# Kernel optimization log

Hardware: AMD Instinct MI355X
Metric: run time of the kernel (lower is better)

Reference implementation:

```python
import jax, jax.numpy as jnp
import numpy as np

N_NODES = 50000
N_EDGES = 640000
D = 128
L = 3
LN_EPS = 1e-5


def _layer_norm(x, g, b):
    mu = jnp.mean(x, axis=-1, keepdims=True)
    var = jnp.mean(jnp.square(x - mu), axis=-1, keepdims=True)
    return (x - mu) * jax.lax.rsqrt(var + LN_EPS) * g + b


def setup_inputs() -> dict:
    key = jax.random.key(0)
    ks = jax.random.split(key, 8)
    scale = 1.0 / np.sqrt(D)
    x = jax.random.normal(ks[0], (N_NODES, D), dtype=jnp.float32)
    edge_index = jax.random.randint(ks[1], (2, N_EDGES), 0, N_NODES, dtype=jnp.int32)
    return {
        "x": x,
        "edge_index": edge_index,
        "eps": jnp.zeros((L,), jnp.float32),  # GIN epsilon, init 0.0
        "W1": jax.random.normal(ks[2], (L, D, D), jnp.float32) * scale,
        "b1": jnp.zeros((L, D), jnp.float32),
        "W2": jax.random.normal(ks[3], (L, D, D), jnp.float32) * scale,
        "b2": jnp.zeros((L, D), jnp.float32),
        "ln_g": jnp.ones((L, D), jnp.float32),   # per-conv LayerNorm
        "ln_b": jnp.zeros((L, D), jnp.float32),
        "skip_g": jnp.ones((L - 1, D), jnp.float32),  # outer norms for layers 0..L-2
        "skip_b": jnp.zeros((L - 1, D), jnp.float32),
    }


def reference(x, edge_index, eps, W1, b1, W2, b2, ln_g, ln_b, skip_g, skip_b):
    src = edge_index[0]
    dst = edge_index[1]
    h = x  # no input_norm (use_input_norm=False)
    for i in range(L):
        h_in = h
        # scatter-add neighbor aggregation: out[dst] += h[src]
        agg = jax.ops.segment_sum(h[src], dst, num_segments=N_NODES)
        z = (1.0 + eps[i]) * h + agg
        # 2-layer MLP: Linear -> ReLU -> Linear
        z = jnp.maximum(z @ W1[i] + b1[i], 0.0) @ W2[i] + b2[i]
        z = _layer_norm(z, ln_g[i], ln_b[i])
        if i < L - 1:
            z = _layer_norm(z, skip_g[i], skip_b[i])  # skip-path norm
            z = jnp.maximum(z, 0.0)  # ReLU; dropout is identity in eval
        h = z + h_in  # residual (shapes always match: in==hidden)
    return h
```

## Files before the change

### kernel.cpp

```cpp
#include <hip/hip_runtime.h>
#include <hip/hip_bf16.h>

#define N_NODES 50000
#define N_EDGES 640000
#define D 128
#define NPAD 50048
#define LAYERS 3
#define SCAN_NB 196

typedef __attribute__((ext_vector_type(4))) float f32x4;
typedef __attribute__((ext_vector_type(8))) short bf16x8;
typedef __attribute__((ext_vector_type(4))) short bf16x4;

static __device__ __forceinline__ short f2bf(float f) {
    union { float f; unsigned u; } x; x.f = f;
    unsigned r = x.u + 0x7fffu + ((x.u >> 16) & 1u);
    return (short)(r >> 16);
}
static __device__ __forceinline__ float bf2f(short s) {
    union { unsigned u; float f; } x; x.u = ((unsigned)(unsigned short)s) << 16;
    return x.f;
}

__global__ void init_kernel(const f32x4* __restrict__ in, bf16x4* __restrict__ hb) {
    int t = blockIdx.x * 256 + threadIdx.x;
    f32x4 v = in[t];
    bf16x4 p; p[0] = f2bf(v.x); p[1] = f2bf(v.y); p[2] = f2bf(v.z); p[3] = f2bf(v.w);
    hb[t] = p;
}

__global__ void prepw_kernel(const float* __restrict__ W1, const float* __restrict__ W2,
                             short* __restrict__ wt) {
    int t = blockIdx.x * 256 + threadIdx.x;
    if (t >= 6 * 16384) return;
    int m = t >> 14, rem = t & 16383;
    int c = rem >> 7, k = rem & 127;
    const float* src = (m < 3) ? (W1 + m * 16384) : (W2 + (m - 3) * 16384);
    wt[m * 16384 + c * 128 + k] = f2bf(src[k * 128 + c]);
}

__global__ void hist_kernel(const int* __restrict__ dst, int* __restrict__ deg) {
    int e = blockIdx.x * 256 + threadIdx.x;
    if (e < N_EDGES) atomicAdd(&deg[dst[e]], 1);
}

__global__ void scan1_kernel(const int* __restrict__ deg, int* __restrict__ rs,
                             int* __restrict__ bsum) {
    __shared__ int tmp[256];
    int i = blockIdx.x * 256 + threadIdx.x;
    int v = (i < N_NODES) ? deg[i] : 0;
    tmp[threadIdx.x] = v;
    __syncthreads();
    for (int off = 1; off < 256; off <<= 1) {
        int t = (threadIdx.x >= off) ? tmp[threadIdx.x - off] : 0;
        __syncthreads();
        tmp[threadIdx.x] += t;
        __syncthreads();
    }
    if (i < N_NODES) rs[i] = tmp[threadIdx.x] - v;
    if (threadIdx.x == 255) bsum[blockIdx.x] = tmp[255];
}

__global__ void scan2_kernel(int* __restrict__ bsum) {
    __shared__ int tmp[256];
    int v = (threadIdx.x < SCAN_NB) ? bsum[threadIdx.x] : 0;
    tmp[threadIdx.x] = v;
    __syncthreads();
    for (int off = 1; off < 256; off <<= 1) {
        int t = (threadIdx.x >= off) ? tmp[threadIdx.x - off] : 0;
        __syncthreads();
        tmp[threadIdx.x] += t;
        __syncthreads();
    }
    if (threadIdx.x < SCAN_NB) bsum[threadIdx.x] = tmp[threadIdx.x] - v;
}

__global__ void scan3_kernel(int* __restrict__ rs, const int* __restrict__ bsum) {
    int i = blockIdx.x * 256 + threadIdx.x;
    if (i < N_NODES) rs[i] += bsum[blockIdx.x];
}

__global__ void fill_kernel(const int* __restrict__ src, const int* __restrict__ dst,
                            const int* __restrict__ rs, int* __restrict__ cursor,
                            int* __restrict__ col) {
    int e = blockIdx.x * 256 + threadIdx.x;
    if (e >= N_EDGES) return;
    int d = dst[e];
    int p = atomicAdd(&cursor[d], 1);
    col[rs[d] + p] = src[e];
}

__global__ __launch_bounds__(256) void agg_kernel(const bf16x8* __restrict__ hb,
                                                  const int* __restrict__ rs,
                                                  const int* __restrict__ deg,
                                                  const int* __restrict__ col,
                                                  const float* __restrict__ epsArr, int layer,
                                                  bf16x8* __restrict__ z) {
    int t = blockIdx.x * 256 + threadIdx.x;
    int node = t >> 4, lane = t & 15;
    if (node >= NPAD) return;
    bf16x8 o;
    if (node < N_NODES) {
        float acc[8] = {0.f, 0.f, 0.f, 0.f, 0.f, 0.f, 0.f, 0.f};
        int start = rs[node], dg = deg[node];
        const int* cp = col + start;
        int base = 0;
        for (; base + 4 <= dg; base += 4) {
            int c0 = cp[base], c1 = cp[base + 1], c2 = cp[base + 2], c3 = cp[base + 3];
            bf16x8 v0 = hb[(size_t)c0 * 16 + lane];
            bf16x8 v1 = hb[(size_t)c1 * 16 + lane];
            bf16x8 v2 = hb[(size_t)c2 * 16 + lane];
            bf16x8 v3 = hb[(size_t)c3 * 16 + lane];
#pragma unroll
            for (int e = 0; e < 8; ++e)
                acc[e] += (bf2f(v0[e]) + bf2f(v1[e])) + (bf2f(v2[e]) + bf2f(v3[e]));
        }
        for (; base < dg; ++base) {
            bf16x8 v = hb[(size_t)cp[base] * 16 + lane];
#pragma unroll
            for (int e = 0; e < 8; ++e) acc[e] += bf2f(v[e]);
        }
        float s = 1.0f + epsArr[layer];
        bf16x8 hv = hb[(size_t)node * 16 + lane];
#pragma unroll
        for (int e = 0; e < 8; ++e) o[e] = f2bf(fmaf(s, bf2f(hv[e]), acc[e]));
    } else {
        o = (bf16x8)(short)0;
    }
    z[(size_t)node * 16 + lane] = o;
}

template <bool LAST>
__global__ __launch_bounds__(256, 2) void mlp_kernel(const short* __restrict__ Z,
                                                     const short* __restrict__ Wt1,
                                                     const float* __restrict__ B1,
                                                     const short* __restrict__ Wt2,
                                                     const float* __restrict__ B2,
                                                     const float* __restrict__ G1,
                                                     const float* __restrict__ Bt1,
                                                     const float* __restrict__ G2,
                                                     const float* __restrict__ Bt2,
                                                     const float* __restrict__ RS,
                                                     float* __restrict__ H,
                                                     short* __restrict__ HB) {
    __shared__ __align__(16) char lds[49152 + 3072];
    const int t = threadIdx.x;
    const int wave = t >> 6, lane = t & 63;
    const int r = lane & 15, kq = lane >> 4;
    const int lrow = wave * 16 + r;
    const int row = blockIdx.x * 64 + lrow;
    const int swzr = (r & 7) << 4;
    const int swzl = (lrow & 7) << 4;
    const int fcol = kq * 16;

    const short* Zr = Z + (size_t)row * D + kq * 8;
    bf16x8 zb0 = *(const bf16x8*)(Zr);
    bf16x8 zb1 = *(const bf16x8*)(Zr + 32);
    bf16x8 zb2 = *(const bf16x8*)(Zr + 64);
    bf16x8 zb3 = *(const bf16x8*)(Zr + 96);
    __builtin_amdgcn_sched_barrier(0);

    bf16x8 g2[8];
    {
        bf16x8 g1[8];
#pragma unroll
        for (int i = 0; i < 8; ++i) g1[i] = *(const bf16x8*)(Wt1 + i * 2048 + t * 8);
#pragma unroll
        for (int i = 0; i < 8; ++i) g2[i] = *(const bf16x8*)(Wt2 + i * 2048 + t * 8);
        if (t < (LAST ? 128 : 192)) {
            int which = t >> 5, chunk = t & 31;
            const float* vp = (which == 0) ? B1 : (which == 1) ? B2 : (which == 2) ? G1
                            : (which == 3) ? Bt1 : (which == 4) ? G2 : Bt2;
            *(f32x4*)(lds + 49152 + which * 512 + chunk * 16) = *(const f32x4*)(vp + chunk * 4);
        }
#pragma unroll
        for (int i = 0; i < 8; ++i) {
            int b = i * 4096 + t * 16;
            *(bf16x8*)(lds + (b ^ (((b >> 8) & 7) << 4))) = g1[i];
        }
    }
    __syncthreads();

    bf16x4 p[8];
#pragma unroll
    for (int ct = 0; ct < 8; ++ct) {
        int wb = (ct * 16 + r) * 256 + kq * 16;
        f32x4 acc = {0.f, 0.f, 0.f, 0.f};
        acc = __builtin_amdgcn_mfma_f32_16x16x32_bf16(*(const bf16x8*)(lds + ((wb      ) ^ swzr)), zb0, acc, 0, 0, 0);
        acc = __builtin_amdgcn_mfma_f32_16x16x32_bf16(*(const bf16x8*)(lds + ((wb +  64) ^ swzr)), zb1, acc, 0, 0, 0);
        acc = __builtin_amdgcn_mfma_f32_16x16x32_bf16(*(const bf16x8*)(lds + ((wb + 128) ^ swzr)), zb2, acc, 0, 0, 0);
        acc = __builtin_amdgcn_mfma_f32_16x16x32_bf16(*(const bf16x8*)(lds + ((wb + 192) ^ swzr)), zb3, acc, 0, 0, 0);
        f32x4 bias = *(const f32x4*)(lds + 49152 + 0 + ct * 64 + fcol);
        p[ct][0] = f2bf(fmaxf(acc[0] + bias.x, 0.0f));
        p[ct][1] = f2bf(fmaxf(acc[1] + bias.y, 0.0f));
        p[ct][2] = f2bf(fmaxf(acc[2] + bias.z, 0.0f));
        p[ct][3] = f2bf(fmaxf(acc[3] + bias.w, 0.0f));
    }
    __syncthreads();

    f32x4 rsv[8] = {};
    if (row < N_NODES) {
#pragma unroll
        for (int ct = 0; ct < 8; ++ct)
            rsv[ct] = *(const f32x4*)(RS + (size_t)row * D + ct * 16 + kq * 4);
    }
    __builtin_amdgcn_sched_barrier(0);

#pragma unroll
    for (int i = 0; i < 8; ++i) {
        int b = i * 4096 + t * 16;
        *(bf16x8*)(lds + (b ^ (((b >> 8) & 7) << 4))) = g2[i];
    }
#pragma unroll
    for (int ct = 0; ct < 8; ++ct)
        *(bf16x4*)(lds + 32768 + ((lrow * 256 + ct * 32 + kq * 8) ^ swzl)) = p[ct];
    __syncthreads();

    bf16x8 hb0 = *(const bf16x8*)(lds + 32768 + ((lrow * 256 +   0 + kq * 16) ^ swzl));
    bf16x8 hb1 = *(const bf16x8*)(lds + 32768 + ((lrow * 256 +  64 + kq * 16) ^ swzl));
    bf16x8 hb2 = *(const bf16x8*)(lds + 32768 + ((lrow * 256 + 128 + kq * 16) ^ swzl));
    bf16x8 hb3 = *(const bf16x8*)(lds + 32768 + ((lrow * 256 + 192 + kq * 16) ^ swzl));

    f32x4 o[8];
#pragma unroll
    for (int ct = 0; ct < 8; ++ct) {
        int wb = (ct * 16 + r) * 256 + kq * 16;
        f32x4 acc = {0.f, 0.f, 0.f, 0.f};
        acc = __builtin_amdgcn_mfma_f32_16x16x32_bf16(*(const bf16x8*)(lds + ((wb      ) ^ swzr)), hb0, acc, 0, 0, 0);
        acc = __builtin_amdgcn_mfma_f32_16x16x32_bf16(*(const bf16x8*)(lds + ((wb +  64) ^ swzr)), hb1, acc, 0, 0, 0);
        acc = __builtin_amdgcn_mfma_f32_16x16x32_bf16(*(const bf16x8*)(lds + ((wb + 128) ^ swzr)), hb2, acc, 0, 0, 0);
        acc = __builtin_amdgcn_mfma_f32_16x16x32_bf16(*(const bf16x8*)(lds + ((wb + 192) ^ swzr)), hb3, acc, 0, 0, 0);
        f32x4 bias = *(const f32x4*)(lds + 49152 + 512 + ct * 64 + fcol);
        o[ct] = acc + bias;
    }

    float s = 0.f, q = 0.f;
#pragma unroll
    for (int ct = 0; ct < 8; ++ct) {
        s += o[ct].x + o[ct].y + o[ct].z + o[ct].w;
        q += o[ct].x * o[ct].x + o[ct].y * o[ct].y + o[ct].z * o[ct].z + o[ct].w * o[ct].w;
    }
    s += __shfl_xor(s, 16, 64); q += __shfl_xor(q, 16, 64);
    s += __shfl_xor(s, 32, 64); q += __shfl_xor(q, 32, 64);
    float mu = s * (1.0f / D);
    float rstd = rsqrtf(q * (1.0f / D) - mu * mu + 1e-5f);
#pragma unroll
    for (int ct = 0; ct < 8; ++ct) {
        f32x4 g = *(const f32x4*)(lds + 49152 + 1024 + ct * 64 + fcol);
        f32x4 b = *(const f32x4*)(lds + 49152 + 1536 + ct * 64 + fcol);
        o[ct] = (o[ct] - mu) * rstd * g + b;
    }

    if (!LAST) {
        float s2 = 0.f, q2 = 0.f;
#pragma unroll
        for (int ct = 0; ct < 8; ++ct) {
            s2 += o[ct].x + o[ct].y + o[ct].z + o[ct].w;
            q2 += o[ct].x * o[ct].x + o[ct].y * o[ct].y + o[ct].z * o[ct].z + o[ct].w * o[ct].w;
        }
        s2 += __shfl_xor(s2, 16, 64); q2 += __shfl_xor(q2, 16, 64);
        s2 += __shfl_xor(s2, 32, 64); q2 += __shfl_xor(q2, 32, 64);
        float mu2 = s2 * (1.0f / D);
        float rstd2 = rsqrtf(q2 * (1.0f / D) - mu2 * mu2 + 1e-5f);
#pragma unroll
        for (int ct = 0; ct < 8; ++ct) {
            f32x4 g = *(const f32x4*)(lds + 49152 + 2048 + ct * 64 + fcol);
            f32x4 b = *(const f32x4*)(lds + 49152 + 2560 + ct * 64 + fcol);
            f32x4 y = (o[ct] - mu2) * rstd2 * g + b;
            y.x = fmaxf(y.x, 0.f); y.y = fmaxf(y.y, 0.f);
            y.z = fmaxf(y.z, 0.f); y.w = fmaxf(y.w, 0.f);
            o[ct] = y;
        }
    }

    if (row < N_NODES) {
#pragma unroll
        for (int ct = 0; ct < 8; ++ct) {
            size_t off = (size_t)row * D + ct * 16 + kq * 4;
            f32x4 hv = rsv[ct] + o[ct];
            *(f32x4*)(H + off) = hv;
            if (!LAST) {
                bf16x4 pb;
                pb[0] = f2bf(hv.x); pb[1] = f2bf(hv.y); pb[2] = f2bf(hv.z); pb[3] = f2bf(hv.w);
                *(bf16x4*)(HB + off) = pb;
            }
        }
    }
}

extern "C" void kernel_launch(void* const* d_in, const int* in_sizes, int n_in,
                              void* d_out, int out_size, void* d_ws, size_t ws_size,
                              hipStream_t stream) {
    const float* x   = (const float*)d_in[0];
    const int*   ei  = (const int*)d_in[1];
    const float* eps = (const float*)d_in[2];
    const float* W1  = (const float*)d_in[3];
    const float* b1  = (const float*)d_in[4];
    const float* W2  = (const float*)d_in[5];
    const float* b2  = (const float*)d_in[6];
    const float* lng = (const float*)d_in[7];
    const float* lnb = (const float*)d_in[8];
    const float* skg = (const float*)d_in[9];
    const float* skb = (const float*)d_in[10];
    float* h = (float*)d_out;

    char* ws = (char*)d_ws;
    short* zbuf = (short*)ws;
    short* hbb  = (short*)(ws + 12812288);
    short* wt   = (short*)(ws + 25624576);
    int*   rs   = (int*)  (ws + 25821184);
    int*   deg  = (int*)  (ws + 26021376);
    int*   cur  = (int*)  (ws + 26221568);
    int*   col  = (int*)  (ws + 26421760);
    int*   bsum = (int*)  (ws + 28981760);

    const int* srcIdx = ei;
    const int* dstIdx = ei + N_EDGES;

    init_kernel<<<(N_NODES * 32) / 256, 256, 0, stream>>>((const f32x4*)x, (bf16x4*)hbb);
    prepw_kernel<<<(6 * 16384) / 256, 256, 0, stream>>>(W1, W2, wt);

    hipMemsetAsync(deg, 0, 2 * 200192, stream);
    hist_kernel<<<(N_EDGES + 255) / 256, 256, 0, stream>>>(dstIdx, deg);
    scan1_kernel<<<SCAN_NB, 256, 0, stream>>>(deg, rs, bsum);
    scan2_kernel<<<1, 256, 0, stream>>>(bsum);
    scan3_kernel<<<SCAN_NB, 256, 0, stream>>>(rs, bsum);
    fill_kernel<<<(N_EDGES + 255) / 256, 256, 0, stream>>>(srcIdx, dstIdx, rs, cur, col);

    for (int l = 0; l < LAYERS; ++l) {
        agg_kernel<<<NPAD / 16, 256, 0, stream>>>(
            (const bf16x8*)hbb, rs, deg, col, eps, l, (bf16x8*)zbuf);
        const float* rsrc = (l == 0) ? x : h;
        if (l < LAYERS - 1) {
            mlp_kernel<false><<<NPAD / 64, 256, 0, stream>>>(
                zbuf, wt + l * 16384, b1 + l * D, wt + (3 + l) * 16384, b2 + l * D,
                lng + l * D, lnb + l * D, skg + l * D, skb + l * D, rsrc, h, hbb);
        } else {
            mlp_kernel<true><<<NPAD / 64, 256, 0, stream>>>(
                zbuf, wt + l * 16384, b1 + l * D, wt + (3 + l) * 16384, b2 + l * D,
                lng + l * D, lnb + l * D, nullptr, nullptr, rsrc, h, nullptr);
        }
    }
}
```

Measured before the change: 224.4 us.

## Split bf16 node features into four column slabs for cache-local gather

Node features and aggregation output now live in four 32-column slabs instead of full 128-column rows. Consecutive aggregation blocks are interleaved across slabs, each handling one slab for 64 nodes with four lanes per node. This is meant to shrink the working set of random neighbor gathers so more of each slab stays in L2/MALL. The gather loop is also unrolled to eight neighbors. The cost is four separate gathers of col and rs/deg per node, and producer/consumer kernels that write and read the strided slab layout.

After: 226.7 us. About the same (+1.0%).

```diff
diff --git a/kernel.cpp b/kernel.cpp
--- a/kernel.cpp
+++ b/kernel.cpp
@@ -8,6 +8,9 @@
 #define LAYERS 3
 #define SCAN_NB 196
 
+#define SLAB_HB (N_NODES * 32)
+#define SLAB_Z  (NPAD * 32)
+
 typedef __attribute__((ext_vector_type(4))) float f32x4;
 typedef __attribute__((ext_vector_type(8))) short bf16x8;
 typedef __attribute__((ext_vector_type(4))) short bf16x4;
@@ -22,11 +25,18 @@
     return x.f;
 }
 
-__global__ void init_kernel(const f32x4* __restrict__ in, bf16x4* __restrict__ hb) {
+__global__ void init_kernel(const float* __restrict__ x, short* __restrict__ hb) {
     int t = blockIdx.x * 256 + threadIdx.x;
-    f32x4 v = in[t];
-    bf16x4 p; p[0] = f2bf(v.x); p[1] = f2bf(v.y); p[2] = f2bf(v.z); p[3] = f2bf(v.w);
-    hb[t] = p;
+    if (t >= N_NODES * 16) return;
+    int node = t >> 4, fg = t & 15;
+    int s = fg >> 2, w = (fg & 3) * 8;
+    const float* xp = x + (size_t)node * D + fg * 8;
+    f32x4 a = *(const f32x4*)(xp);
+    f32x4 b = *(const f32x4*)(xp + 4);
+    bf16x8 p;
+    p[0] = f2bf(a.x); p[1] = f2bf(a.y); p[2] = f2bf(a.z); p[3] = f2bf(a.w);
+    p[4] = f2bf(b.x); p[5] = f2bf(b.y); p[6] = f2bf(b.z); p[7] = f2bf(b.w);
+    *(bf16x8*)(hb + (size_t)s * SLAB_HB + (size_t)node * 32 + w) = p;
 }
 
 __global__ void prepw_kernel(const float* __restrict__ W1, const float* __restrict__ W2,
@@ -90,44 +100,53 @@
     col[rs[d] + p] = src[e];
 }
 
-__global__ __launch_bounds__(256) void agg_kernel(const bf16x8* __restrict__ hb,
+__global__ __launch_bounds__(256) void agg_kernel(const short* __restrict__ hb,
                                                   const int* __restrict__ rs,
                                                   const int* __restrict__ deg,
                                                   const int* __restrict__ col,
                                                   const float* __restrict__ epsArr, int layer,
-                                                  bf16x8* __restrict__ z) {
-    int t = blockIdx.x * 256 + threadIdx.x;
-    int node = t >> 4, lane = t & 15;
-    if (node >= NPAD) return;
+                                                  short* __restrict__ z) {
+    int b = blockIdx.x;
+    int j = b & 7, m = b >> 3;
+    int slice = j & 3;
+    int chunk = 2 * m + (j >> 2);
+    int t = threadIdx.x;
+    int g = t >> 2, lane4 = t & 3;
+    int node = chunk * 64 + g;
+    const short* tab = hb + (size_t)slice * SLAB_HB;
     bf16x8 o;
     if (node < N_NODES) {
         float acc[8] = {0.f, 0.f, 0.f, 0.f, 0.f, 0.f, 0.f, 0.f};
         int start = rs[node], dg = deg[node];
         const int* cp = col + start;
         int base = 0;
-        for (; base + 4 <= dg; base += 4) {
-            int c0 = cp[base], c1 = cp[base + 1], c2 = cp[base + 2], c3 = cp[base + 3];
-            bf16x8 v0 = hb[(size_t)c0 * 16 + lane];
-            bf16x8 v1 = hb[(size_t)c1 * 16 + lane];
-            bf16x8 v2 = hb[(size_t)c2 * 16 + lane];
-            bf16x8 v3 = hb[(size_t)c3 * 16 + lane];
+        for (; base + 8 <= dg; base += 8) {
+            bf16x8 v0 = *(const bf16x8*)(tab + (size_t)cp[base + 0] * 32 + lane4 * 8);
+            bf16x8 v1 = *(const bf16x8*)(tab + (size_t)cp[base + 1] * 32 + lane4 * 8);
+            bf16x8 v2 = *(const bf16x8*)(tab + (size_t)cp[base + 2] * 32 + lane4 * 8);
+            bf16x8 v3 = *(const bf16x8*)(tab + (size_t)cp[base + 3] * 32 + lane4 * 8);
+            bf16x8 v4 = *(const bf16x8*)(tab + (size_t)cp[base + 4] * 32 + lane4 * 8);
+            bf16x8 v5 = *(const bf16x8*)(tab + (size_t)cp[base + 5] * 32 + lane4 * 8);
+            bf16x8 v6 = *(const bf16x8*)(tab + (size_t)cp[base + 6] * 32 + lane4 * 8);
+            bf16x8 v7 = *(const bf16x8*)(tab + (size_t)cp[base + 7] * 32 + lane4 * 8);
 #pragma unroll
             for (int e = 0; e < 8; ++e)
-                acc[e] += (bf2f(v0[e]) + bf2f(v1[e])) + (bf2f(v2[e]) + bf2f(v3[e]));
+                acc[e] += ((bf2f(v0[e]) + bf2f(v1[e])) + (bf2f(v2[e]) + bf2f(v3[e])))
+                        + ((bf2f(v4[e]) + bf2f(v5[e])) + (bf2f(v6[e]) + bf2f(v7[e])));
         }
         for (; base < dg; ++base) {
-            bf16x8 v = hb[(size_t)cp[base] * 16 + lane];
+            bf16x8 v = *(const bf16x8*)(tab + (size_t)cp[base] * 32 + lane4 * 8);
 #pragma unroll
             for (int e = 0; e < 8; ++e) acc[e] += bf2f(v[e]);
         }
         float s = 1.0f + epsArr[layer];
-        bf16x8 hv = hb[(size_t)node * 16 + lane];
+        bf16x8 hv = *(const bf16x8*)(tab + (size_t)node * 32 + lane4 * 8);
 #pragma unroll
         for (int e = 0; e < 8; ++e) o[e] = f2bf(fmaf(s, bf2f(hv[e]), acc[e]));
     } else {
         o = (bf16x8)(short)0;
     }
-    z[(size_t)node * 16 + lane] = o;
+    *(bf16x8*)(z + (size_t)slice * SLAB_Z + (size_t)node * 32 + lane4 * 8) = o;
 }
 
 template <bool LAST>
@@ -153,11 +172,10 @@
     const int swzl = (lrow & 7) << 4;
     const int fcol = kq * 16;
 
-    const short* Zr = Z + (size_t)row * D + kq * 8;
-    bf16x8 zb0 = *(const bf16x8*)(Zr);
-    bf16x8 zb1 = *(const bf16x8*)(Zr + 32);
-    bf16x8 zb2 = *(const bf16x8*)(Zr + 64);
-    bf16x8 zb3 = *(const bf16x8*)(Zr + 96);
+    bf16x8 zb0 = *(const bf16x8*)(Z + (size_t)0 * SLAB_Z + (size_t)row * 32 + kq * 8);
+    bf16x8 zb1 = *(const bf16x8*)(Z + (size_t)1 * SLAB_Z + (size_t)row * 32 + kq * 8);
+    bf16x8 zb2 = *(const bf16x8*)(Z + (size_t)2 * SLAB_Z + (size_t)row * 32 + kq * 8);
+    bf16x8 zb3 = *(const bf16x8*)(Z + (size_t)3 * SLAB_Z + (size_t)row * 32 + kq * 8);
     __builtin_amdgcn_sched_barrier(0);
 
     bf16x8 g2[8];
@@ -282,7 +300,9 @@
             if (!LAST) {
                 bf16x4 pb;
                 pb[0] = f2bf(hv.x); pb[1] = f2bf(hv.y); pb[2] = f2bf(hv.z); pb[3] = f2bf(hv.w);
-                *(bf16x4*)(HB + off) = pb;
+                int sl = ct >> 1;
+                int w = (ct & 1) * 16 + kq * 4;
+                *(bf16x4*)(HB + (size_t)sl * SLAB_HB + (size_t)row * 32 + w) = pb;
             }
         }
     }
@@ -307,17 +327,17 @@
     char* ws = (char*)d_ws;
     short* zbuf = (short*)ws;
     short* hbb  = (short*)(ws + 12812288);
-    short* wt   = (short*)(ws + 25624576);
-    int*   rs   = (int*)  (ws + 25821184);
-    int*   deg  = (int*)  (ws + 26021376);
-    int*   cur  = (int*)  (ws + 26221568);
-    int*   col  = (int*)  (ws + 26421760);
-    int*   bsum = (int*)  (ws + 28981760);
+    short* wt   = (short*)(ws + 25612288);
+    int*   rs   = (int*)  (ws + 25808896);
+    int*   deg  = (int*)  (ws + 26009088);
+    int*   cur  = (int*)  (ws + 26209280);
+    int*   col  = (int*)  (ws + 26409472);
+    int*   bsum = (int*)  (ws + 28969472);
 
     const int* srcIdx = ei;
     const int* dstIdx = ei + N_EDGES;
 
-    init_kernel<<<(N_NODES * 32) / 256, 256, 0, stream>>>((const f32x4*)x, (bf16x4*)hbb);
+    init_kernel<<<(N_NODES * 16 + 255) / 256, 256, 0, stream>>>(x, hbb);
     prepw_kernel<<<(6 * 16384) / 256, 256, 0, stream>>>(W1, W2, wt);
 
     hipMemsetAsync(deg, 0, 2 * 200192, stream);
@@ -328,8 +348,8 @@
     fill_kernel<<<(N_EDGES + 255) / 256, 256, 0, stream>>>(srcIdx, dstIdx, rs, cur, col);
 
     for (int l = 0; l < LAYERS; ++l) {
-        agg_kernel<<<NPAD / 16, 256, 0, stream>>>(
-            (const bf16x8*)hbb, rs, deg, col, eps, l, (bf16x8*)zbuf);
+        agg_kernel<<<391 * 8, 256, 0, stream>>>(
+            hbb, rs, deg, col, eps, l, zbuf);
         const float* rsrc = (l == 0) ? x : h;
         if (l < LAYERS - 1) {
             mlp_kernel<false><<<NPAD / 64, 256, 0, stream>>>(
```
